# Kernel tuning notes

Hardware: AMD Instinct MI355X
Metric: run time of the kernel (lower is better)

The kernel has to match this reference:

```python
import jax, jax.numpy as jnp
import numpy as np

N_NODES, N_EDGES, F_IN, C, L = 20000, 320000, 128, 300, 8


def _gru_cell(m, h, w_ih, w_hh, b_ih, b_hh):
    # torch.nn.GRUCell math; gate chunk order: reset, update, new
    gi = m @ w_ih.T + b_ih            # [N, 3C]
    gh = h @ w_hh.T + b_hh            # [N, 3C]
    i_r, i_z, i_n = jnp.split(gi, 3, axis=-1)
    h_r, h_z, h_n = jnp.split(gh, 3, axis=-1)
    r = jax.nn.sigmoid(i_r + h_r)
    z = jax.nn.sigmoid(i_z + h_z)
    n = jnp.tanh(i_n + r * h_n)
    return (1.0 - z) * n + z * h


def _gated_graph_conv(x, src, dst, W, w_ih, w_hh, b_ih, b_hh):
    # PyG GatedGraphConv: zero-pad input to out_channels, then L steps of
    # (linear -> scatter-add over edges j->i -> GRUCell update).
    N = x.shape[0]
    out_ch = W.shape[-1]
    if x.shape[1] < out_ch:
        x = jnp.pad(x, ((0, 0), (0, out_ch - x.shape[1])))
    for i in range(W.shape[0]):  # fixed small L; weights differ per step
        m = x @ W[i]                                   # [N, C]
        agg = jax.ops.segment_sum(m[src], dst, num_segments=N)  # add-aggr
        x = _gru_cell(agg, x, w_ih, w_hh, b_ih, b_hh)
    return x


def setup_inputs() -> dict:
    key = jax.random.key(0)
    ks = jax.random.split(key, 12)
    s = 0.05  # keep activations in the non-saturating range of sigmoid/tanh
    return {
        "x": jax.random.normal(ks[0], (N_NODES, F_IN), jnp.float32),
        "edge_index": jax.random.randint(ks[1], (2, N_EDGES), 0, N_NODES, jnp.int32),
        "W1": jax.random.normal(ks[2], (L, C, C), jnp.float32) * s,
        "gru1_wih": jax.random.normal(ks[3], (3 * C, C), jnp.float32) * s,
        "gru1_whh": jax.random.normal(ks[4], (3 * C, C), jnp.float32) * s,
        "gru1_bih": jax.random.normal(ks[5], (3 * C,), jnp.float32) * s,
        "gru1_bhh": jax.random.normal(ks[6], (3 * C,), jnp.float32) * s,
        "W2": jax.random.normal(ks[7], (L, C, C), jnp.float32) * s,
        "gru2_wih": jax.random.normal(ks[8], (3 * C, C), jnp.float32) * s,
        "gru2_whh": jax.random.normal(ks[9], (3 * C, C), jnp.float32) * s,
        "gru2_bih": jax.random.normal(ks[10], (3 * C,), jnp.float32) * s,
        "gru2_bhh": jax.random.normal(ks[11], (3 * C,), jnp.float32) * s,
    }


def reference(x, edge_index, W1, gru1_wih, gru1_whh, gru1_bih, gru1_bhh,
              W2, gru2_wih, gru2_whh, gru2_bih, gru2_bhh):
    src, dst = edge_index[0], edge_index[1]
    h = _gated_graph_conv(x, src, dst, W1, gru1_wih, gru1_whh, gru1_bih, gru1_bhh)
    h = jax.nn.relu(h)
    # F.dropout(training=self.training) is identity in eval mode
    h = _gated_graph_conv(h, src, dst, W2, gru2_wih, gru2_whh, gru2_bih, gru2_bhh)
    pooled = jnp.mean(h, axis=0)           # [C]
    return jax.nn.log_softmax(pooled)[None, :]  # [1, C]
```

## Files before the change

kernel.cpp:

```cpp
#include <hip/hip_runtime.h>
#include <math.h>

#define N_NODES 20000
#define N_EDGES 320000
#define F_IN 128
#define C 300
#define L_STEPS 8
#define KP 320
#define SP 328
#define NPAD 304
#define GOFS 97280
#define WSTEP 291840
#define LOSCALE 2048.0f

typedef _Float16 half8 __attribute__((ext_vector_type(8)));
typedef _Float16 half4 __attribute__((ext_vector_type(4)));
typedef __attribute__((ext_vector_type(4))) float floatx4;

__device__ __forceinline__ void split16(float x, _Float16& hi, _Float16& lo) {
    hi = (_Float16)x;
    lo = (_Float16)((x - (float)hi) * LOSCALE);
}

__global__ void pad_kernel(const float* __restrict__ x, float* __restrict__ h,
                           _Float16* __restrict__ hh, _Float16* __restrict__ hl) {
    int idx = blockIdx.x * blockDim.x + threadIdx.x;
    if (idx >= N_NODES * KP) return;
    int n = idx / KP, c = idx - n * KP;
    float v = (c < F_IN) ? x[n * F_IN + c] : 0.0f;
    if (c < C) h[(size_t)n * C + c] = v;
    _Float16 hi, lo; split16(v, hi, lo);
    hh[idx] = hi; hl[idx] = lo;
}

__global__ void hist_kernel(const int* __restrict__ dst, int* __restrict__ deg) {
    int e = blockIdx.x * blockDim.x + threadIdx.x;
    if (e < N_EDGES) atomicAdd(&deg[dst[e]], 1);
}

__global__ void scan_kernel(const int* __restrict__ deg, int* __restrict__ row_ptr) {
    __shared__ int part[1024];
    const int PER = 20;
    int t = threadIdx.x;
    int base = t * PER;
    int vals[PER];
    int s = 0;
    #pragma unroll
    for (int i = 0; i < PER; ++i) {
        int idx = base + i;
        int v = (idx < N_NODES) ? deg[idx] : 0;
        vals[i] = s; s += v;
    }
    part[t] = s;
    __syncthreads();
    for (int off = 1; off < 1024; off <<= 1) {
        int v = (t >= off) ? part[t - off] : 0;
        __syncthreads();
        part[t] += v;
        __syncthreads();
    }
    int pre = (t == 0) ? 0 : part[t - 1];
    #pragma unroll
    for (int i = 0; i < PER; ++i) {
        int idx = base + i;
        if (idx < N_NODES) row_ptr[idx] = pre + vals[i];
    }
    if (t == 0) row_ptr[N_NODES] = N_EDGES;
}

__global__ void cursor_copy(const int* __restrict__ row_ptr, int* __restrict__ cur) {
    int i = blockIdx.x * blockDim.x + threadIdx.x;
    if (i < N_NODES) cur[i] = row_ptr[i];
}

__global__ void fill_kernel(const int* __restrict__ src, const int* __restrict__ dst,
                            int* __restrict__ cur, int* __restrict__ colx) {
    int e = blockIdx.x * blockDim.x + threadIdx.x;
    if (e >= N_EDGES) return;
    int d = dst[e];
    int p = atomicAdd(&cur[d], 1);
    colx[p] = src[e];
}

__launch_bounds__(256)
__global__ void wcomb_split(const float* __restrict__ W1, const float* __restrict__ W2,
                            const float* __restrict__ wih1, const float* __restrict__ wih2,
                            _Float16* __restrict__ whi, _Float16* __restrict__ wlo) {
    int z = blockIdx.z, layer = z >> 3, step = z & 7;
    const float* A  = (layer ? W2 : W1) + (size_t)step * C * C;
    const float* Bm = layer ? wih2 : wih1;
    _Float16* ohi = whi + (size_t)z * WSTEP;
    _Float16* olo = wlo + (size_t)z * WSTEP;
    __shared__ float As[16][68];
    __shared__ float Bs[16][68];
    int tid = threadIdx.x;
    int tx = tid & 15, ty = tid >> 4;
    int rowBase = blockIdx.y * 64, colBase = blockIdx.x * 64;
    float acc[4][4] = {};
    int lr = tid >> 2, k4 = (tid & 3) * 4;
    for (int k0 = 0; k0 < C; k0 += 16) {
        {
            int gr = rowBase + lr;
            int gn = colBase + lr;
            #pragma unroll
            for (int j = 0; j < 4; ++j) {
                int k = k0 + k4 + j;
                As[k4 + j][lr] = (gr < C && k < C) ? A[(size_t)gr * C + k] : 0.f;
                Bs[k4 + j][lr] = (gn < 3 * C && k < C) ? Bm[(size_t)gn * C + k] : 0.f;
            }
        }
        __syncthreads();
        #pragma unroll
        for (int k = 0; k < 16; ++k) {
            float4 a = *(const float4*)&As[k][ty * 4];
            float4 b = *(const float4*)&Bs[k][tx * 4];
            float av[4] = {a.x, a.y, a.z, a.w};
            float bv[4] = {b.x, b.y, b.z, b.w};
            #pragma unroll
            for (int i = 0; i < 4; ++i)
                #pragma unroll
                for (int j = 0; j < 4; ++j)
                    acc[i][j] += av[i] * bv[j];
        }
        __syncthreads();
    }
    #pragma unroll
    for (int i = 0; i < 4; ++i) {
        int r = rowBase + ty * 4 + i;
        if (r >= C) continue;
        #pragma unroll
        for (int j = 0; j < 4; ++j) {
            int gn = colBase + tx * 4 + j;
            if (gn >= 3 * C) continue;
            int g = (gn >= 2 * C) ? 2 : ((gn >= C) ? 1 : 0);
            int n = gn - g * C;
            size_t idx = (((size_t)g * 40 + (r >> 3)) * NPAD + n) * 8 + (r & 7);
            _Float16 hi, lo; split16(acc[i][j], hi, lo);
            ohi[idx] = hi; olo[idx] = lo;
        }
    }
}

__global__ void whh_split(const float* __restrict__ whh1, const float* __restrict__ whh2,
                          _Float16* __restrict__ whi, _Float16* __restrict__ wlo) {
    int idx = blockIdx.x * blockDim.x + threadIdx.x;
    if (idx >= 2 * 3 * C * C) return;
    int k = idx % C;
    int rest = idx / C;
    int gn = rest % (3 * C);
    int layer = rest / (3 * C);
    int g = (gn >= 2 * C) ? 2 : ((gn >= C) ? 1 : 0);
    int n = gn - g * C;
    float v = (layer ? whh2 : whh1)[(size_t)gn * C + k];
    size_t o = (size_t)layer * WSTEP + (((size_t)g * 40 + (k >> 3)) * NPAD + n) * 8 + (k & 7);
    _Float16 hi, lo; split16(v, hi, lo);
    whi[o] = hi; wlo[o] = lo;
}

__global__ void aggregate_kernel(const float* __restrict__ h,
                                 const int* __restrict__ rowp,
                                 const int* __restrict__ colx,
                                 _Float16* __restrict__ agh, _Float16* __restrict__ agl) {
    const int node = blockIdx.x * 4 + (threadIdx.x >> 6);
    const int lane = threadIdx.x & 63;
    const int beg = rowp[node], end = rowp[node + 1];
    float4 a0 = make_float4(0.f, 0.f, 0.f, 0.f);
    float4 a1 = make_float4(0.f, 0.f, 0.f, 0.f);
    const bool tail = lane < 11;
    for (int e = beg; e < end; ++e) {
        const float* row = h + (size_t)colx[e] * C;
        float4 v = *(const float4*)&row[lane * 4];
        a0.x += v.x; a0.y += v.y; a0.z += v.z; a0.w += v.w;
        if (tail) {
            float4 u = *(const float4*)&row[(64 + lane) * 4];
            a1.x += u.x; a1.y += u.y; a1.z += u.z; a1.w += u.w;
        }
    }
    half4 vh, vl;
    {
        _Float16 hi, lo;
        split16(a0.x, hi, lo); vh[0] = hi; vl[0] = lo;
        split16(a0.y, hi, lo); vh[1] = hi; vl[1] = lo;
        split16(a0.z, hi, lo); vh[2] = hi; vl[2] = lo;
        split16(a0.w, hi, lo); vh[3] = hi; vl[3] = lo;
    }
    _Float16* oh = agh + (size_t)node * KP;
    _Float16* ol = agl + (size_t)node * KP;
    *(half4*)&oh[lane * 4] = vh;
    *(half4*)&ol[lane * 4] = vl;
    if (tail) {
        _Float16 hi, lo;
        split16(a1.x, hi, lo); vh[0] = hi; vl[0] = lo;
        split16(a1.y, hi, lo); vh[1] = hi; vl[1] = lo;
        split16(a1.z, hi, lo); vh[2] = hi; vl[2] = lo;
        split16(a1.w, hi, lo); vh[3] = hi; vl[3] = lo;
        *(half4*)&oh[(64 + lane) * 4] = vh;
        *(half4*)&ol[(64 + lane) * 4] = vl;
    }
}

struct BFrag { half8 v[12]; };
__device__ __forceinline__ BFrag load_bfrags(const _Float16* __restrict__ wch,
                                             const _Float16* __restrict__ wcl,
                                             const _Float16* __restrict__ whh_,
                                             const _Float16* __restrict__ whl_,
                                             int kc, int ncol) {
    BFrag f;
    const size_t bofs = ((size_t)kc * NPAD + ncol) * 8;
    f.v[0]  = *(const half8*)&wch[bofs];
    f.v[1]  = *(const half8*)&wch[GOFS + bofs];
    f.v[2]  = *(const half8*)&wch[2 * GOFS + bofs];
    f.v[3]  = *(const half8*)&wcl[bofs];
    f.v[4]  = *(const half8*)&wcl[GOFS + bofs];
    f.v[5]  = *(const half8*)&wcl[2 * GOFS + bofs];
    f.v[6]  = *(const half8*)&whh_[bofs];
    f.v[7]  = *(const half8*)&whh_[GOFS + bofs];
    f.v[8]  = *(const half8*)&whh_[2 * GOFS + bofs];
    f.v[9]  = *(const half8*)&whl_[bofs];
    f.v[10] = *(const half8*)&whl_[GOFS + bofs];
    f.v[11] = *(const half8*)&whl_[2 * GOFS + bofs];
    return f;
}

#define MFMA16(A, B, ACC) __builtin_amdgcn_mfma_f32_16x16x32_f16(A, B, ACC, 0, 0, 0)

#define MFMA_SUB(aR1, aR2, aZ1, aZ2, aN1, aN2, aH1, aH2, GH, GL, AH, AL, B)  \
    aR1 = MFMA16(GH, B.v[0],  aR1);                                          \
    aZ1 = MFMA16(GH, B.v[1],  aZ1);                                          \
    aN1 = MFMA16(GH, B.v[2],  aN1);                                          \
    aR2 = MFMA16(GH, B.v[3],  aR2);                                          \
    aZ2 = MFMA16(GH, B.v[4],  aZ2);                                          \
    aN2 = MFMA16(GH, B.v[5],  aN2);                                          \
    aR2 = MFMA16(GL, B.v[0],  aR2);                                          \
    aZ2 = MFMA16(GL, B.v[1],  aZ2);                                          \
    aN2 = MFMA16(GL, B.v[2],  aN2);                                          \
    aR1 = MFMA16(AH, B.v[6],  aR1);                                          \
    aZ1 = MFMA16(AH, B.v[7],  aZ1);                                          \
    aH1 = MFMA16(AH, B.v[8],  aH1);                                          \
    aR2 = MFMA16(AH, B.v[9],  aR2);                                          \
    aZ2 = MFMA16(AH, B.v[10], aZ2);                                          \
    aH2 = MFMA16(AH, B.v[11], aH2);                                          \
    aR2 = MFMA16(AL, B.v[6],  aR2);                                          \
    aZ2 = MFMA16(AL, B.v[7],  aZ2);                                          \
    aH2 = MFMA16(AL, B.v[8],  aH2);

__attribute__((amdgpu_flat_work_group_size(256, 256), amdgpu_waves_per_eu(2, 2)))
__global__ void gru_f16(_Float16* __restrict__ hh, _Float16* __restrict__ hl,
                        const _Float16* __restrict__ agh, const _Float16* __restrict__ agl,
                        const _Float16* __restrict__ wch, const _Float16* __restrict__ wcl,
                        const _Float16* __restrict__ whh_, const _Float16* __restrict__ whl_,
                        const float* __restrict__ bih, const float* __restrict__ bhh,
                        float* __restrict__ h) {
    __shared__ _Float16 Lhh[32 * SP];
    __shared__ _Float16 Lhl[32 * SP];
    __shared__ _Float16 Lgh[32 * SP];
    const int tid = threadIdx.x;
    const int rowBase = blockIdx.x * 32;
    {
        int r = tid >> 3, c8 = tid & 7;
        const _Float16* ph = hh + (size_t)(rowBase + r) * KP;
        const _Float16* pl = hl + (size_t)(rowBase + r) * KP;
        const _Float16* pg = agh + (size_t)(rowBase + r) * KP;
        #pragma unroll
        for (int i = 0; i < 5; ++i) {
            int k = (c8 + i * 8) * 8;
            *(int4*)&Lhh[r * SP + k] = *(const int4*)&ph[k];
            *(int4*)&Lhl[r * SP + k] = *(const int4*)&pl[k];
            *(int4*)&Lgh[r * SP + k] = *(const int4*)&pg[k];
        }
    }
    __syncthreads();
    const int lane = tid & 63, w = tid >> 6;
    const int quad = lane >> 4, n15 = lane & 15;
    const int arow0 = n15;
    const int arow1 = 16 + n15;
    const _Float16* pgl0 = agl + (size_t)(rowBase + arow0) * KP + quad * 8;
    const _Float16* pgl1 = agl + (size_t)(rowBase + arow1) * KP + quad * 8;

    for (int ct = w; ct < 19; ct += 4) {
        floatx4 R1s0, R2s0, Z1s0, Z2s0, N1s0, N2s0, H1s0, H2s0;
        floatx4 R1s1, R2s1, Z1s1, Z2s1, N1s1, N2s1, H1s1, H2s1;
        R1s0 = R2s0 = Z1s0 = Z2s0 = N1s0 = N2s0 = H1s0 = H2s0 = (floatx4){0.f,0.f,0.f,0.f};
        R1s1 = R2s1 = Z1s1 = Z2s1 = N1s1 = N2s1 = H1s1 = H2s1 = (floatx4){0.f,0.f,0.f,0.f};
        const int ncol = ct * 16 + n15;
        BFrag B0 = load_bfrags(wch, wcl, whh_, whl_, quad, ncol);
        half8 GA0 = *(const half8*)&pgl0[0];
        half8 GA1 = *(const half8*)&pgl1[0];
        BFrag B1;
        half8 GB0, GB1;
        #pragma unroll
        for (int kt = 0; kt < 10; ++kt) {
            if (kt < 9) {
                const int kn = kt + 1;
                if (kt & 1) {
                    B0  = load_bfrags(wch, wcl, whh_, whl_, kn * 4 + quad, ncol);
                    GA0 = *(const half8*)&pgl0[kn * 32];
                    GA1 = *(const half8*)&pgl1[kn * 32];
                } else {
                    B1  = load_bfrags(wch, wcl, whh_, whl_, kn * 4 + quad, ncol);
                    GB0 = *(const half8*)&pgl0[kn * 32];
                    GB1 = *(const half8*)&pgl1[kn * 32];
                }
            }
            const BFrag& B  = (kt & 1) ? B1 : B0;
            const half8 GL0 = (kt & 1) ? GB0 : GA0;
            const half8 GL1 = (kt & 1) ? GB1 : GA1;
            const int ko = kt * 32 + quad * 8;
            half8 GH0 = *(const half8*)&Lgh[arow0 * SP + ko];
            half8 AH0 = *(const half8*)&Lhh[arow0 * SP + ko];
            half8 AL0 = *(const half8*)&Lhl[arow0 * SP + ko];
            half8 GH1 = *(const half8*)&Lgh[arow1 * SP + ko];
            half8 AH1 = *(const half8*)&Lhh[arow1 * SP + ko];
            half8 AL1 = *(const half8*)&Lhl[arow1 * SP + ko];
            __builtin_amdgcn_sched_barrier(0);
            __builtin_amdgcn_s_setprio(1);
            MFMA_SUB(R1s0, R2s0, Z1s0, Z2s0, N1s0, N2s0, H1s0, H2s0,
                     GH0, GL0, AH0, AL0, B)
            MFMA_SUB(R1s1, R2s1, Z1s1, Z2s1, N1s1, N2s1, H1s1, H2s1,
                     GH1, GL1, AH1, AL1, B)
            __builtin_amdgcn_s_setprio(0);
        }
        const int col = ncol;
        if (col < C) {
            const float invS = 1.0f / LOSCALE;
            const float rbias = bih[col] + bhh[col];
            const float zbias = bih[C + col] + bhh[C + col];
            const float nbias = bih[2 * C + col];
            const float hbias = bhh[2 * C + col];
            #pragma unroll
            for (int i = 0; i < 4; ++i) {
                int grow = rowBase + quad * 4 + i;
                float rr  = R1s0[i] + R2s0[i] * invS + rbias;
                float zz  = Z1s0[i] + Z2s0[i] * invS + zbias;
                float inn = N1s0[i] + N2s0[i] * invS + nbias;
                float hn  = H1s0[i] + H2s0[i] * invS + hbias;
                float r = 1.f / (1.f + __expf(-rr));
                float z = 1.f / (1.f + __expf(-zz));
                float nn = tanhf(inn + r * hn);
                float hold = h[(size_t)grow * C + col];
                float hnew = (1.f - z) * nn + z * hold;
                h[(size_t)grow * C + col] = hnew;
                _Float16 nh, nl; split16(hnew, nh, nl);
                hh[(size_t)grow * KP + col] = nh;
                hl[(size_t)grow * KP + col] = nl;
            }
            #pragma unroll
            for (int i = 0; i < 4; ++i) {
                int grow = rowBase + 16 + quad * 4 + i;
                float rr  = R1s1[i] + R2s1[i] * invS + rbias;
                float zz  = Z1s1[i] + Z2s1[i] * invS + zbias;
                float inn = N1s1[i] + N2s1[i] * invS + nbias;
                float hn  = H1s1[i] + H2s1[i] * invS + hbias;
                float r = 1.f / (1.f + __expf(-rr));
                float z = 1.f / (1.f + __expf(-zz));
                float nn = tanhf(inn + r * hn);
                float hold = h[(size_t)grow * C + col];
                float hnew = (1.f - z) * nn + z * hold;
                h[(size_t)grow * C + col] = hnew;
                _Float16 nh, nl; split16(hnew, nh, nl);
                hh[(size_t)grow * KP + col] = nh;
                hl[(size_t)grow * KP + col] = nl;
            }
        }
    }
}

__global__ void relu_kernel(float* __restrict__ h, _Float16* __restrict__ hh,
                            _Float16* __restrict__ hl) {
    int idx = blockIdx.x * blockDim.x + threadIdx.x;
    if (idx >= N_NODES * C) return;
    int n = idx / C, c = idx - n * C;
    float v = fmaxf(h[idx], 0.f);
    h[idx] = v;
    _Float16 hi, lo; split16(v, hi, lo);
    hh[(size_t)n * KP + c] = hi;
    hl[(size_t)n * KP + c] = lo;
}

__global__ void pool_kernel(const float* __restrict__ h, float* __restrict__ pooled) {
    int c = threadIdx.x;
    if (c >= C) return;
    float acc = 0.f;
    for (int n = blockIdx.x; n < N_NODES; n += gridDim.x)
        acc += h[(size_t)n * C + c];
    atomicAdd(&pooled[c], acc);
}

__global__ void lsm_kernel(const float* __restrict__ pooled, float* __restrict__ out) {
    __shared__ float sm[512];
    int t = threadIdx.x;
    float v = (t < C) ? pooled[t] * (1.0f / N_NODES) : -INFINITY;
    sm[t] = v;
    __syncthreads();
    for (int s = 256; s > 0; s >>= 1) {
        if (t < s) sm[t] = fmaxf(sm[t], sm[t + s]);
        __syncthreads();
    }
    float mx = sm[0];
    __syncthreads();
    float e = (t < C) ? expf(v - mx) : 0.f;
    sm[t] = e;
    __syncthreads();
    for (int s = 256; s > 0; s >>= 1) {
        if (t < s) sm[t] += sm[t + s];
        __syncthreads();
    }
    float lse = logf(sm[0]);
    if (t < C) out[t] = (v - mx) - lse;
}

extern "C" void kernel_launch(void* const* d_in, const int* in_sizes, int n_in,
                              void* d_out, int out_size, void* d_ws, size_t ws_size,
                              hipStream_t stream) {
    const float* x      = (const float*)d_in[0];
    const int*   ei     = (const int*)d_in[1];
    const int*   src    = ei;
    const int*   dst    = ei + N_EDGES;
    const float* W1     = (const float*)d_in[2];
    const float* g1_wih = (const float*)d_in[3];
    const float* g1_whh = (const float*)d_in[4];
    const float* g1_bih = (const float*)d_in[5];
    const float* g1_bhh = (const float*)d_in[6];
    const float* W2     = (const float*)d_in[7];
    const float* g2_wih = (const float*)d_in[8];
    const float* g2_whh = (const float*)d_in[9];
    const float* g2_bih = (const float*)d_in[10];
    const float* g2_bhh = (const float*)d_in[11];

    char* p = (char*)d_ws;
    float* h = (float*)p;               p += (size_t)N_NODES * C * 4;
    _Float16* hh = (_Float16*)p;        p += (size_t)N_NODES * KP * 2;
    _Float16* hl = (_Float16*)p;        p += (size_t)N_NODES * KP * 2;
    _Float16* agh = (_Float16*)p;       p += (size_t)N_NODES * KP * 2;
    _Float16* agl = (_Float16*)p;       p += (size_t)N_NODES * KP * 2;
    _Float16* wch = (_Float16*)p;       p += (size_t)16 * WSTEP * 2;
    _Float16* wcl = (_Float16*)p;       p += (size_t)16 * WSTEP * 2;
    _Float16* wh_hi = (_Float16*)p;     p += (size_t)2 * WSTEP * 2;
    _Float16* wh_lo = (_Float16*)p;     p += (size_t)2 * WSTEP * 2;
    float* pooled = (float*)p;          p += 1216;
    int* row_ptr = (int*)p;             p += 80016;
    int* colx = (int*)p;                p += (size_t)N_EDGES * 4;
    int* deg = (int*)p;                 p += 80000;
    int* cursor = (int*)p;              p += 80000;

    hipMemsetAsync(deg, 0, N_NODES * sizeof(int), stream);
    hipMemsetAsync(agh, 0, (size_t)N_NODES * KP * 2, stream);
    hipMemsetAsync(agl, 0, (size_t)N_NODES * KP * 2, stream);
    hipMemsetAsync(wch, 0, (size_t)16 * WSTEP * 2, stream);
    hipMemsetAsync(wcl, 0, (size_t)16 * WSTEP * 2, stream);
    hipMemsetAsync(wh_hi, 0, (size_t)2 * WSTEP * 2, stream);
    hipMemsetAsync(wh_lo, 0, (size_t)2 * WSTEP * 2, stream);
    hipMemsetAsync(pooled, 0, C * sizeof(float), stream);

    pad_kernel<<<(N_NODES * KP + 255) / 256, 256, 0, stream>>>(x, h, hh, hl);

    hist_kernel<<<(N_EDGES + 255) / 256, 256, 0, stream>>>(dst, deg);
    scan_kernel<<<1, 1024, 0, stream>>>(deg, row_ptr);
    cursor_copy<<<(N_NODES + 255) / 256, 256, 0, stream>>>(row_ptr, cursor);
    fill_kernel<<<(N_EDGES + 255) / 256, 256, 0, stream>>>(src, dst, cursor, colx);

    wcomb_split<<<dim3(15, 5, 16), 256, 0, stream>>>(W1, W2, g1_wih, g2_wih, wch, wcl);
    whh_split<<<(2 * 3 * C * C + 255) / 256, 256, 0, stream>>>(g1_whh, g2_whh, wh_hi, wh_lo);

    for (int layer = 0; layer < 2; ++layer) {
        const float* bih = layer ? g2_bih : g1_bih;
        const float* bhh = layer ? g2_bhh : g1_bhh;
        const _Float16* whh_hi = wh_hi + (size_t)layer * WSTEP;
        const _Float16* whh_lo = wh_lo + (size_t)layer * WSTEP;
        for (int step = 0; step < L_STEPS; ++step) {
            const _Float16* wc_hi = wch + (size_t)(layer * 8 + step) * WSTEP;
            const _Float16* wc_lo = wcl + (size_t)(layer * 8 + step) * WSTEP;
            aggregate_kernel<<<N_NODES / 4, 256, 0, stream>>>(h, row_ptr, colx, agh, agl);
            gru_f16<<<N_NODES / 32, 256, 0, stream>>>(
                hh, hl, agh, agl, wc_hi, wc_lo, whh_hi, whh_lo, bih, bhh, h);
        }
        if (layer == 0)
            relu_kernel<<<(N_NODES * C + 255) / 256, 256, 0, stream>>>(h, hh, hl);
    }

    pool_kernel<<<256, 320, 0, stream>>>(h, pooled);
    lsm_kernel<<<1, 512, 0, stream>>>(pooled, (float*)d_out);
}
```

Measured before the change: 3.292 ms.

## Stream GRU weight fragments into LDS with a triple-buffered global_load_lds pipeline

The GRU kernel now stages B-weight fragments through per-wave LDS triple buffers filled by asynchronous global_load_lds, with explicit vmcnt waits, in place of register-held double-buffered global loads. The low half of the aggregated input is also staged into LDS instead of being read from global memory per k-step. Each k-tile is split into gi and gh halves so each buffer holds only six fragments. The aim is to cut register pressure and hide weight-load latency behind MFMAs. In exchange, LDS use grows and occupancy is dropped to one block per CU, and correctness now depends on hand-counted waitcnt values.

```diff
diff --git a/kernel.cpp b/kernel.cpp
--- a/kernel.cpp
+++ b/kernel.cpp
@@ -199,128 +199,170 @@
     }
 }
 
-struct BFrag { half8 v[12]; };
-__device__ __forceinline__ BFrag load_bfrags(const _Float16* __restrict__ wch,
-                                             const _Float16* __restrict__ wcl,
-                                             const _Float16* __restrict__ whh_,
-                                             const _Float16* __restrict__ whl_,
-                                             int kc, int ncol) {
-    BFrag f;
-    const size_t bofs = ((size_t)kc * NPAD + ncol) * 8;
-    f.v[0]  = *(const half8*)&wch[bofs];
-    f.v[1]  = *(const half8*)&wch[GOFS + bofs];
-    f.v[2]  = *(const half8*)&wch[2 * GOFS + bofs];
-    f.v[3]  = *(const half8*)&wcl[bofs];
-    f.v[4]  = *(const half8*)&wcl[GOFS + bofs];
-    f.v[5]  = *(const half8*)&wcl[2 * GOFS + bofs];
-    f.v[6]  = *(const half8*)&whh_[bofs];
-    f.v[7]  = *(const half8*)&whh_[GOFS + bofs];
-    f.v[8]  = *(const half8*)&whh_[2 * GOFS + bofs];
-    f.v[9]  = *(const half8*)&whl_[bofs];
-    f.v[10] = *(const half8*)&whl_[GOFS + bofs];
-    f.v[11] = *(const half8*)&whl_[2 * GOFS + bofs];
-    return f;
-}
-
 #define MFMA16(A, B, ACC) __builtin_amdgcn_mfma_f32_16x16x32_f16(A, B, ACC, 0, 0, 0)
 
-#define MFMA_SUB(aR1, aR2, aZ1, aZ2, aN1, aN2, aH1, aH2, GH, GL, AH, AL, B)  \
-    aR1 = MFMA16(GH, B.v[0],  aR1);                                          \
-    aZ1 = MFMA16(GH, B.v[1],  aZ1);                                          \
-    aN1 = MFMA16(GH, B.v[2],  aN1);                                          \
-    aR2 = MFMA16(GH, B.v[3],  aR2);                                          \
-    aZ2 = MFMA16(GH, B.v[4],  aZ2);                                          \
-    aN2 = MFMA16(GH, B.v[5],  aN2);                                          \
-    aR2 = MFMA16(GL, B.v[0],  aR2);                                          \
-    aZ2 = MFMA16(GL, B.v[1],  aZ2);                                          \
-    aN2 = MFMA16(GL, B.v[2],  aN2);                                          \
-    aR1 = MFMA16(AH, B.v[6],  aR1);                                          \
-    aZ1 = MFMA16(AH, B.v[7],  aZ1);                                          \
-    aH1 = MFMA16(AH, B.v[8],  aH1);                                          \
-    aR2 = MFMA16(AH, B.v[9],  aR2);                                          \
-    aZ2 = MFMA16(AH, B.v[10], aZ2);                                          \
-    aH2 = MFMA16(AH, B.v[11], aH2);                                          \
-    aR2 = MFMA16(AL, B.v[6],  aR2);                                          \
-    aZ2 = MFMA16(AL, B.v[7],  aZ2);                                          \
-    aH2 = MFMA16(AL, B.v[8],  aH2);
-
-__attribute__((amdgpu_flat_work_group_size(256, 256), amdgpu_waves_per_eu(2, 2)))
+#define GLD(srcp, dsto) __builtin_amdgcn_global_load_lds(                      \
+    (const __attribute__((address_space(1))) void*)(srcp),                     \
+    (__attribute__((address_space(3))) void*)(dsto), 16, 0, 0)
+
+__launch_bounds__(256, 1)
 __global__ void gru_f16(_Float16* __restrict__ hh, _Float16* __restrict__ hl,
                         const _Float16* __restrict__ agh, const _Float16* __restrict__ agl,
                         const _Float16* __restrict__ wch, const _Float16* __restrict__ wcl,
                         const _Float16* __restrict__ whh_, const _Float16* __restrict__ whl_,
                         const float* __restrict__ bih, const float* __restrict__ bhh,
                         float* __restrict__ h) {
-    __shared__ _Float16 Lhh[32 * SP];
-    __shared__ _Float16 Lhl[32 * SP];
-    __shared__ _Float16 Lgh[32 * SP];
+    __shared__ _Float16 LDS[41984 + 36864];
+    _Float16* Lgh = LDS;
+    _Float16* Lgl = LDS + 32 * SP;
+    _Float16* Lhh = LDS + 2 * 32 * SP;
+    _Float16* Lhl = LDS + 3 * 32 * SP;
     const int tid = threadIdx.x;
     const int rowBase = blockIdx.x * 32;
     {
         int r = tid >> 3, c8 = tid & 7;
-        const _Float16* ph = hh + (size_t)(rowBase + r) * KP;
-        const _Float16* pl = hl + (size_t)(rowBase + r) * KP;
-        const _Float16* pg = agh + (size_t)(rowBase + r) * KP;
+        const _Float16* pg  = agh + (size_t)(rowBase + r) * KP;
+        const _Float16* pgl = agl + (size_t)(rowBase + r) * KP;
+        const _Float16* ph  = hh  + (size_t)(rowBase + r) * KP;
+        const _Float16* pl  = hl  + (size_t)(rowBase + r) * KP;
         #pragma unroll
         for (int i = 0; i < 5; ++i) {
             int k = (c8 + i * 8) * 8;
+            *(int4*)&Lgh[r * SP + k] = *(const int4*)&pg[k];
+            *(int4*)&Lgl[r * SP + k] = *(const int4*)&pgl[k];
             *(int4*)&Lhh[r * SP + k] = *(const int4*)&ph[k];
             *(int4*)&Lhl[r * SP + k] = *(const int4*)&pl[k];
-            *(int4*)&Lgh[r * SP + k] = *(const int4*)&pg[k];
-        }
-    }
-    __syncthreads();
+        }
+    }
     const int lane = tid & 63, w = tid >> 6;
     const int quad = lane >> 4, n15 = lane & 15;
-    const int arow0 = n15;
-    const int arow1 = 16 + n15;
-    const _Float16* pgl0 = agl + (size_t)(rowBase + arow0) * KP + quad * 8;
-    const _Float16* pgl1 = agl + (size_t)(rowBase + arow1) * KP + quad * 8;
-
-    for (int ct = w; ct < 19; ct += 4) {
-        floatx4 R1s0, R2s0, Z1s0, Z2s0, N1s0, N2s0, H1s0, H2s0;
-        floatx4 R1s1, R2s1, Z1s1, Z2s1, N1s1, N2s1, H1s1, H2s1;
-        R1s0 = R2s0 = Z1s0 = Z2s0 = N1s0 = N2s0 = H1s0 = H2s0 = (floatx4){0.f,0.f,0.f,0.f};
-        R1s1 = R2s1 = Z1s1 = Z2s1 = N1s1 = N2s1 = H1s1 = H2s1 = (floatx4){0.f,0.f,0.f,0.f};
-        const int ncol = ct * 16 + n15;
-        BFrag B0 = load_bfrags(wch, wcl, whh_, whl_, quad, ncol);
-        half8 GA0 = *(const half8*)&pgl0[0];
-        half8 GA1 = *(const half8*)&pgl1[0];
-        BFrag B1;
-        half8 GB0, GB1;
+    const int arow0 = n15, arow1 = 16 + n15;
+    const int lane_ofs = (quad * NPAD + n15) * 8;
+    _Float16* BW = LDS + 41984 + w * 9216;
+
+    const _Float16 *g0 = wch,  *g1 = wch + GOFS,  *g2 = wch + 2 * GOFS;
+    const _Float16 *g3 = wcl,  *g4 = wcl + GOFS,  *g5 = wcl + 2 * GOFS;
+    const _Float16 *q0 = whh_, *q1 = whh_ + GOFS, *q2 = whh_ + 2 * GOFS;
+    const _Float16 *q3 = whl_, *q4 = whl_ + GOFS, *q5 = whl_ + 2 * GOFS;
+
+    auto STAGE_G = [&](int ct2, int kt2, int buf) {
+        const int ko = kt2 * 9728 + ct2 * 128 + lane_ofs;
+        _Float16* d = BW + buf * 3072;
+        GLD(g0 + ko, d);        GLD(g1 + ko, d + 512);  GLD(g2 + ko, d + 1024);
+        GLD(g3 + ko, d + 1536); GLD(g4 + ko, d + 2048); GLD(g5 + ko, d + 2560);
+    };
+    auto STAGE_A = [&](int ct2, int kt2, int buf) {
+        const int ko = kt2 * 9728 + ct2 * 128 + lane_ofs;
+        _Float16* d = BW + buf * 3072;
+        GLD(q0 + ko, d);        GLD(q1 + ko, d + 512);  GLD(q2 + ko, d + 1024);
+        GLD(q3 + ko, d + 1536); GLD(q4 + ko, d + 2048); GLD(q5 + ko, d + 2560);
+    };
+
+    const int nct = (w < 3) ? 5 : 4;
+    STAGE_G(w, 0, 0);
+    STAGE_A(w, 0, 1);
+    STAGE_G(w, 1, 2);
+    __syncthreads();
+
+    int bufc = 0;
+    const int lofs8 = lane * 8;
+    for (int ci = 0; ci < nct; ++ci) {
+        const int ct = w + ci * 4;
+        const bool lastc = (ci == nct - 1);
+        floatx4 R10, R20, Z10, Z20, N10, N20, H10, H20;
+        floatx4 R11, R21, Z11, Z21, N11, N21, H11, H21;
+        R10 = R20 = Z10 = Z20 = N10 = N20 = H10 = H20 = (floatx4){0.f,0.f,0.f,0.f};
+        R11 = R21 = Z11 = Z21 = N11 = N21 = H11 = H21 = (floatx4){0.f,0.f,0.f,0.f};
         #pragma unroll
         for (int kt = 0; kt < 10; ++kt) {
-            if (kt < 9) {
-                const int kn = kt + 1;
-                if (kt & 1) {
-                    B0  = load_bfrags(wch, wcl, whh_, whl_, kn * 4 + quad, ncol);
-                    GA0 = *(const half8*)&pgl0[kn * 32];
-                    GA1 = *(const half8*)&pgl1[kn * 32];
+            #pragma unroll
+            for (int hf = 0; hf < 2; ++hf) {
+                if (kt == 9 && hf == 0) {
+                    if (lastc) asm volatile("s_waitcnt vmcnt(6)" ::: "memory");
+                    else       asm volatile("s_waitcnt vmcnt(12)" ::: "memory");
+                } else if (kt == 9 && hf == 1) {
+                    if (lastc) asm volatile("s_waitcnt vmcnt(0)" ::: "memory");
+                    else       asm volatile("s_waitcnt vmcnt(12)" ::: "memory");
                 } else {
-                    B1  = load_bfrags(wch, wcl, whh_, whl_, kn * 4 + quad, ncol);
-                    GB0 = *(const half8*)&pgl0[kn * 32];
-                    GB1 = *(const half8*)&pgl1[kn * 32];
+                    asm volatile("s_waitcnt vmcnt(12)" ::: "memory");
                 }
+                _Float16* bb = BW + bufc * 3072 + lofs8;
+                half8 b0 = *(const half8*)&bb[0];
+                half8 b1 = *(const half8*)&bb[512];
+                half8 b2 = *(const half8*)&bb[1024];
+                half8 b3 = *(const half8*)&bb[1536];
+                half8 b4 = *(const half8*)&bb[2048];
+                half8 b5 = *(const half8*)&bb[2560];
+                const int ko2 = kt * 32 + quad * 8;
+                half8 X0h, X0l, X1h, X1l;
+                if (hf == 0) {
+                    X0h = *(const half8*)&Lgh[arow0 * SP + ko2];
+                    X0l = *(const half8*)&Lgl[arow0 * SP + ko2];
+                    X1h = *(const half8*)&Lgh[arow1 * SP + ko2];
+                    X1l = *(const half8*)&Lgl[arow1 * SP + ko2];
+                } else {
+                    X0h = *(const half8*)&Lhh[arow0 * SP + ko2];
+                    X0l = *(const half8*)&Lhl[arow0 * SP + ko2];
+                    X1h = *(const half8*)&Lhh[arow1 * SP + ko2];
+                    X1l = *(const half8*)&Lhl[arow1 * SP + ko2];
+                }
+                asm volatile("s_waitcnt lgkmcnt(0)" ::: "memory");
+                __builtin_amdgcn_sched_barrier(0);
+                {
+                    const int sl = kt * 2 + hf + 3;
+                    if (!(lastc && sl >= 20)) {
+                        const int sct = (sl >= 20) ? (ct + 4) : ct;
+                        const int skt = (sl >= 20) ? ((sl - 20) >> 1) : (sl >> 1);
+                        if ((sl & 1) == 0) STAGE_G(sct, skt, bufc);
+                        else               STAGE_A(sct, skt, bufc);
+                    }
+                }
+                __builtin_amdgcn_sched_barrier(0);
+                __builtin_amdgcn_s_setprio(1);
+                if (hf == 0) {
+                    R10 = MFMA16(X0h, b0, R10);
+                    Z10 = MFMA16(X0h, b1, Z10);
+                    N10 = MFMA16(X0h, b2, N10);
+                    R20 = MFMA16(X0h, b3, R20);
+                    Z20 = MFMA16(X0h, b4, Z20);
+                    N20 = MFMA16(X0h, b5, N20);
+                    R20 = MFMA16(X0l, b0, R20);
+                    Z20 = MFMA16(X0l, b1, Z20);
+                    N20 = MFMA16(X0l, b2, N20);
+                    R11 = MFMA16(X1h, b0, R11);
+                    Z11 = MFMA16(X1h, b1, Z11);
+                    N11 = MFMA16(X1h, b2, N11);
+                    R21 = MFMA16(X1h, b3, R21);
+                    Z21 = MFMA16(X1h, b4, Z21);
+                    N21 = MFMA16(X1h, b5, N21);
+                    R21 = MFMA16(X1l, b0, R21);
+                    Z21 = MFMA16(X1l, b1, Z21);
+                    N21 = MFMA16(X1l, b2, N21);
+                } else {
+                    R10 = MFMA16(X0h, b0, R10);
+                    Z10 = MFMA16(X0h, b1, Z10);
+                    H10 = MFMA16(X0h, b2, H10);
+                    R20 = MFMA16(X0h, b3, R20);
+                    Z20 = MFMA16(X0h, b4, Z20);
+                    H20 = MFMA16(X0h, b5, H20);
+                    R20 = MFMA16(X0l, b0, R20);
+                    Z20 = MFMA16(X0l, b1, Z20);
+                    H20 = MFMA16(X0l, b2, H20);
+                    R11 = MFMA16(X1h, b0, R11);
+                    Z11 = MFMA16(X1h, b1, Z11);
+                    H11 = MFMA16(X1h, b2, H11);
+                    R21 = MFMA16(X1h, b3, R21);
+                    Z21 = MFMA16(X1h, b4, Z21);
+                    H21 = MFMA16(X1h, b5, H21);
+                    R21 = MFMA16(X1l, b0, R21);
+                    Z21 = MFMA16(X1l, b1, Z21);
+                    H21 = MFMA16(X1l, b2, H21);
+                }
+                __builtin_amdgcn_s_setprio(0);
+                bufc = (bufc == 2) ? 0 : bufc + 1;
             }
-            const BFrag& B  = (kt & 1) ? B1 : B0;
-            const half8 GL0 = (kt & 1) ? GB0 : GA0;
-            const half8 GL1 = (kt & 1) ? GB1 : GA1;
-            const int ko = kt * 32 + quad * 8;
-            half8 GH0 = *(const half8*)&Lgh[arow0 * SP + ko];
-            half8 AH0 = *(const half8*)&Lhh[arow0 * SP + ko];
-            half8 AL0 = *(const half8*)&Lhl[arow0 * SP + ko];
-            half8 GH1 = *(const half8*)&Lgh[arow1 * SP + ko];
-            half8 AH1 = *(const half8*)&Lhh[arow1 * SP + ko];
-            half8 AL1 = *(const half8*)&Lhl[arow1 * SP + ko];
-            __builtin_amdgcn_sched_barrier(0);
-            __builtin_amdgcn_s_setprio(1);
-            MFMA_SUB(R1s0, R2s0, Z1s0, Z2s0, N1s0, N2s0, H1s0, H2s0,
-                     GH0, GL0, AH0, AL0, B)
-            MFMA_SUB(R1s1, R2s1, Z1s1, Z2s1, N1s1, N2s1, H1s1, H2s1,
-                     GH1, GL1, AH1, AL1, B)
-            __builtin_amdgcn_s_setprio(0);
-        }
-        const int col = ncol;
+        }
+        const int col = ct * 16 + n15;
         if (col < C) {
             const float invS = 1.0f / LOSCALE;
             const float rbias = bih[col] + bhh[col];
@@ -330,10 +372,10 @@
             #pragma unroll
             for (int i = 0; i < 4; ++i) {
                 int grow = rowBase + quad * 4 + i;
-                float rr  = R1s0[i] + R2s0[i] * invS + rbias;
-                float zz  = Z1s0[i] + Z2s0[i] * invS + zbias;
-                float inn = N1s0[i] + N2s0[i] * invS + nbias;
-                float hn  = H1s0[i] + H2s0[i] * invS + hbias;
+                float rr  = R10[i] + R20[i] * invS + rbias;
+                float zz  = Z10[i] + Z20[i] * invS + zbias;
+                float inn = N10[i] + N20[i] * invS + nbias;
+                float hn  = H10[i] + H20[i] * invS + hbias;
                 float r = 1.f / (1.f + __expf(-rr));
                 float z = 1.f / (1.f + __expf(-zz));
                 float nn = tanhf(inn + r * hn);
@@ -347,10 +389,10 @@
             #pragma unroll
             for (int i = 0; i < 4; ++i) {
                 int grow = rowBase + 16 + quad * 4 + i;
-                float rr  = R1s1[i] + R2s1[i] * invS + rbias;
-                float zz  = Z1s1[i] + Z2s1[i] * invS + zbias;
-                float inn = N1s1[i] + N2s1[i] * invS + nbias;
-                float hn  = H1s1[i] + H2s1[i] * invS + hbias;
+                float rr  = R11[i] + R21[i] * invS + rbias;
+                float zz  = Z11[i] + Z21[i] * invS + zbias;
+                float inn = N11[i] + N21[i] * invS + nbias;
+                float hn  = H11[i] + H21[i] * invS + hbias;
                 float r = 1.f / (1.f + __expf(-rr));
                 float z = 1.f / (1.f + __expf(-zz));
                 float nn = tanhf(inn + r * hn);
```

Result: slower. 3.564 ms (+8.3%).
